# Performance work log

Hardware: AMD Instinct MI355X
Metric: run time of the kernel (lower is better)

The kernel has to match this reference:

```python
import jax, jax.numpy as jnp
import numpy as np

N_HEAD = 16
N_EMBD = 1024
TIME_EMBD = 64
EPS = 1e-5

def _ln(x, w, b):
    mu = jnp.mean(x, axis=-1, keepdims=True)
    var = jnp.mean(jnp.square(x - mu), axis=-1, keepdims=True)
    return (x - mu) * jax.lax.rsqrt(var + EPS) * w + b

def _gelu(x):
    return jax.nn.gelu(x, approximate=False)

def setup_inputs() -> dict:
    key = jax.random.key(0)
    ks = jax.random.split(key, 12)
    B, T, D, TE = 2, 2048, N_EMBD, TIME_EMBD
    C = D + TE  # 1088
    s = lambda fan_in: 1.0 / np.sqrt(fan_in)
    return {
        "z": jax.random.normal(ks[0], (B, T, D), jnp.float32),
        "t": jax.random.uniform(ks[1], (B,), jnp.float32),
        # time_mlp: Linear(1, TE) -> GELU -> Linear(TE, TE)
        "w_t1": jax.random.normal(ks[2], (1, TE), jnp.float32) * s(1),
        "b_t1": jnp.zeros((TE,), jnp.float32),
        "w_t2": jax.random.normal(ks[3], (TE, TE), jnp.float32) * s(TE),
        "b_t2": jnp.zeros((TE,), jnp.float32),
        # attention
        "ln_a_w": jnp.ones((C,), jnp.float32),
        "ln_a_b": jnp.zeros((C,), jnp.float32),
        "w_attn": jax.random.normal(ks[4], (C, 3 * D), jnp.float32) * s(C),
        "b_attn": jnp.zeros((3 * D,), jnp.float32),
        "w_proj": jax.random.normal(ks[5], (D, D), jnp.float32) * s(D),
        "b_proj": jnp.zeros((D,), jnp.float32),
        # mlp
        "ln_m_w": jnp.ones((C,), jnp.float32),
        "ln_m_b": jnp.zeros((C,), jnp.float32),
        "w_fc": jax.random.normal(ks[6], (C, 4 * D), jnp.float32) * s(C),
        "b_fc": jnp.zeros((4 * D,), jnp.float32),
        "w_fc2": jax.random.normal(ks[7], (4 * D, D), jnp.float32) * s(4 * D),
        "b_fc2": jnp.zeros((D,), jnp.float32),
    }

def reference(z, t, w_t1, b_t1, w_t2, b_t2, ln_a_w, ln_a_b, w_attn, b_attn,
              w_proj, b_proj, ln_m_w, ln_m_b, w_fc, b_fc, w_fc2, b_fc2):
    B, T, D = z.shape
    H, hd = N_HEAD, N_EMBD // N_HEAD
    # time embedding: [B, TE] broadcast over T
    t_emb = _gelu(t[:, None] @ w_t1 + b_t1) @ w_t2 + b_t2
    t_emb_bt = jnp.broadcast_to(t_emb[:, None, :], (B, T, TIME_EMBD))
    # --- attention with time-conditioned input ---
    zt = jnp.concatenate([z, t_emb_bt], axis=-1)            # [B,T,D+TE]
    x = _ln(zt, ln_a_w, ln_a_b)
    qkv = x @ w_attn + b_attn                               # [B,T,3D]
    q, k, v = jnp.split(qkv, 3, axis=-1)
    q = q.reshape(B, T, H, hd)
    k = k.reshape(B, T, H, hd)
    v = v.reshape(B, T, H, hd)
    att = jnp.einsum('bqhd,bkhd->bhqk', q, k) * (1.0 / np.sqrt(hd))
    mask = jnp.tril(jnp.ones((T, T), bool))
    att = jnp.where(mask, att, -jnp.inf)
    att = jax.nn.softmax(att, axis=-1)
    y = jnp.einsum('bhqk,bkhd->bqhd', att, v).reshape(B, T, D)
    h = y @ w_proj + b_proj                                 # [B,T,D]
    # --- mlp with time-conditioned input ---
    ht = jnp.concatenate([h, t_emb_bt], axis=-1)
    m = _ln(ht, ln_m_w, ln_m_b)
    dz = _gelu(m @ w_fc + b_fc) @ w_fc2 + b_fc2             # [B,T,D]
    return dz
```

## Files before the change

kernel.cpp:

```cpp
#include <hip/hip_runtime.h>
#include <stdint.h>
#include <math.h>

#define T_SEQ 2048
#define NHEAD 16
#define HD 64
#define DMODEL 1024
#define CDIM 1088
#define MROWS 4096

typedef uint16_t u16;
typedef __bf16 b8v __attribute__((ext_vector_type(8)));
typedef float f4v __attribute__((ext_vector_type(4)));

typedef __attribute__((address_space(3))) void lds_void;
typedef const __attribute__((address_space(1))) void glb_void;

__device__ __forceinline__ float b2f(u16 u) {
  union { uint32_t i; float f; } c; c.i = ((uint32_t)u) << 16; return c.f;
}
__device__ __forceinline__ u16 f2b(float f) {
  union { float f; uint32_t i; } c; c.f = f;
  uint32_t x = c.i;
  return (u16)((x + 0x7fffu + ((x >> 16) & 1u)) >> 16);
}
__device__ __forceinline__ float gelu_f(float x) {
  float ax = fabsf(x);
  float xs = ax * 0.70710678118654752f;
  float t = __frcp_rn(1.0f + 0.3275911f * xs);
  float poly = ((((1.061405429f * t - 1.453152027f) * t + 1.421413741f) * t
                 - 0.284496736f) * t + 0.254829592f) * t;
  float e = __expf(-xs * xs);
  float er = 1.0f - poly * e;
  er = copysignf(er, x);
  return 0.5f * x * (1.0f + er);
}

__global__ void time_mlp_kernel(const float* __restrict__ t, const float* __restrict__ w1,
                                const float* __restrict__ b1, const float* __restrict__ w2,
                                const float* __restrict__ b2, float* __restrict__ temb) {
  __shared__ float h1[2][64];
  int tid = threadIdx.x;
  int b = tid >> 6, i = tid & 63;
  float tv = t[b];
  h1[b][i] = gelu_f(tv * w1[i] + b1[i]);
  __syncthreads();
  float acc = b2[i];
  for (int k = 0; k < 64; ++k) acc += h1[b][k] * w2[k * 64 + i];
  temb[b * 64 + i] = acc;
}

__global__ __launch_bounds__(256) void transpose_kernel(const float* __restrict__ src,
                                                        u16* __restrict__ dst,
                                                        int R, int C) {
  __shared__ u16 tile[32][33];
  int tx = threadIdx.x & 31, ty = threadIdx.x >> 5;
  int c0 = blockIdx.x * 32, r0 = blockIdx.y * 32;
#pragma unroll
  for (int i = 0; i < 4; ++i) {
    int r = ty + i * 8;
    tile[r][tx] = f2b(src[(size_t)(r0 + r) * C + c0 + tx]);
  }
  __syncthreads();
#pragma unroll
  for (int i = 0; i < 4; ++i) {
    int c = ty + i * 8;
    dst[(size_t)(c0 + c) * R + r0 + tx] = tile[tx][c];
  }
}

__global__ __launch_bounds__(256) void add2_kernel(const float4* __restrict__ a,
                                                   const float4* __restrict__ b,
                                                   float4* __restrict__ o, int n4) {
  int i = blockIdx.x * 256 + threadIdx.x;
  if (i < n4) {
    float4 x = a[i], y = b[i];
    o[i] = float4{x.x + y.x, x.y + y.y, x.z + y.z, x.w + y.w};
  }
}

__global__ __launch_bounds__(256) void ln_concat_kernel(const float* __restrict__ zf,
                                                        const float* __restrict__ zf2,
                                                        const u16* __restrict__ zb,
                                                        const float* __restrict__ temb,
                                                        const float* __restrict__ w,
                                                        const float* __restrict__ bvec,
                                                        u16* __restrict__ xout,
                                                        int mode) {
  __shared__ float red[4];
  int row = blockIdx.x;
  int b = row / T_SEQ;
  int tid = threadIdx.x;
  float v[5];
  float sum = 0.f;
#pragma unroll
  for (int i = 0; i < 5; ++i) {
    int c = tid + i * 256;
    float val = 0.f;
    if (c < CDIM) {
      if (c < DMODEL) {
        size_t idx = (size_t)row * DMODEL + c;
        if (mode == 0) val = b2f(zb[idx]);
        else if (mode == 1) val = zf[idx];
        else val = zf[idx] + zf2[idx];
      } else {
        val = temb[b * 64 + (c - DMODEL)];
      }
    }
    v[i] = val;
    sum += val;
  }
#pragma unroll
  for (int off = 32; off; off >>= 1) sum += __shfl_xor(sum, off, 64);
  int wv = tid >> 6, ln = tid & 63;
  if (ln == 0) red[wv] = sum;
  __syncthreads();
  float mean = (red[0] + red[1] + red[2] + red[3]) * (1.0f / CDIM);
  __syncthreads();
  float sq = 0.f;
#pragma unroll
  for (int i = 0; i < 5; ++i) {
    int c = tid + i * 256;
    if (c < CDIM) { float d = v[i] - mean; sq += d * d; }
  }
#pragma unroll
  for (int off = 32; off; off >>= 1) sq += __shfl_xor(sq, off, 64);
  if (ln == 0) red[wv] = sq;
  __syncthreads();
  float inv = rsqrtf((red[0] + red[1] + red[2] + red[3]) * (1.0f / CDIM) + 1e-5f);
#pragma unroll
  for (int i = 0; i < 5; ++i) {
    int c = tid + i * 256;
    if (c < CDIM)
      xout[(size_t)row * CDIM + c] = f2b((v[i] - mean) * inv * w[c] + bvec[c]);
  }
}

__global__ __launch_bounds__(256) void gemm_bt_kernel(const u16* __restrict__ A,
                                                      const u16* __restrict__ Bt,
                                                      const float* __restrict__ bias,
                                                      void* __restrict__ Cout,
                                                      int M, int N, int K,
                                                      int do_gelu, int out_f32) {
  __shared__ u16 As[2][128 * 32];
  __shared__ u16 Bs[2][128 * 32];
  const int tid = threadIdx.x;
  const int wave = tid >> 6, lane = tid & 63;
  const int wr = wave >> 1, wc = wave & 1;
  const int m0 = blockIdx.x * 128;
  const int n0 = blockIdx.y * 128;
  const int lrow = lane & 15, quad = lane >> 4;
  const int srow = lane >> 2, sseg = lane & 3;

  const u16* gA0 = A  + (size_t)(m0 + wave * 32 + srow) * K + sseg * 8;
  const u16* gA1 = gA0 + (size_t)16 * K;
  const u16* gB0 = Bt + (size_t)(n0 + wave * 32 + srow) * K + sseg * 8;
  const u16* gB1 = gB0 + (size_t)16 * K;
  const int la0 = (wave * 32) * 32, la1 = (wave * 32 + 16) * 32;

  f4v acc[4][4] = {};

  __builtin_amdgcn_global_load_lds((glb_void*)gA0, (lds_void*)&As[0][la0], 16, 0, 0);
  __builtin_amdgcn_global_load_lds((glb_void*)gA1, (lds_void*)&As[0][la1], 16, 0, 0);
  __builtin_amdgcn_global_load_lds((glb_void*)gB0, (lds_void*)&Bs[0][la0], 16, 0, 0);
  __builtin_amdgcn_global_load_lds((glb_void*)gB1, (lds_void*)&Bs[0][la1], 16, 0, 0);

  int cur = 0;
  for (int k0 = 0; k0 < K; k0 += 32) {
    __syncthreads();
    if (k0 + 32 < K) {
      int nxt = cur ^ 1;
      __builtin_amdgcn_global_load_lds((glb_void*)(gA0 + k0 + 32), (lds_void*)&As[nxt][la0], 16, 0, 0);
      __builtin_amdgcn_global_load_lds((glb_void*)(gA1 + k0 + 32), (lds_void*)&As[nxt][la1], 16, 0, 0);
      __builtin_amdgcn_global_load_lds((glb_void*)(gB0 + k0 + 32), (lds_void*)&Bs[nxt][la0], 16, 0, 0);
      __builtin_amdgcn_global_load_lds((glb_void*)(gB1 + k0 + 32), (lds_void*)&Bs[nxt][la1], 16, 0, 0);
    }
    b8v af[4], bfr[4];
#pragma unroll
    for (int mi = 0; mi < 4; ++mi)
      af[mi] = *(const b8v*)(&As[cur][(wr * 64 + mi * 16 + lrow) * 32 + quad * 8]);
#pragma unroll
    for (int ni = 0; ni < 4; ++ni)
      bfr[ni] = *(const b8v*)(&Bs[cur][(wc * 64 + ni * 16 + lrow) * 32 + quad * 8]);
#pragma unroll
    for (int mi = 0; mi < 4; ++mi)
#pragma unroll
      for (int ni = 0; ni < 4; ++ni)
        acc[mi][ni] = __builtin_amdgcn_mfma_f32_16x16x32_bf16(bfr[ni], af[mi], acc[mi][ni], 0, 0, 0);
    cur ^= 1;
  }

#pragma unroll
  for (int mi = 0; mi < 4; ++mi) {
    int grow = m0 + wr * 64 + mi * 16 + lrow;
    size_t rb = (size_t)grow * N;
#pragma unroll
    for (int ni = 0; ni < 4; ++ni) {
      int gcol = n0 + wc * 64 + ni * 16 + quad * 4;
      float4 bv = *(const float4*)(bias + gcol);
      float v0 = acc[mi][ni][0] + bv.x;
      float v1 = acc[mi][ni][1] + bv.y;
      float v2 = acc[mi][ni][2] + bv.z;
      float v3 = acc[mi][ni][3] + bv.w;
      if (do_gelu) {
        v0 = gelu_f(v0); v1 = gelu_f(v1); v2 = gelu_f(v2); v3 = gelu_f(v3);
      }
      if (out_f32) {
        *(float4*)((float*)Cout + rb + gcol) = float4{v0, v1, v2, v3};
      } else {
        ushort4 ov;
        ov.x = f2b(v0); ov.y = f2b(v1); ov.z = f2b(v2); ov.w = f2b(v3);
        *(ushort4*)((u16*)Cout + rb + gcol) = ov;
      }
    }
  }
}

__global__ __launch_bounds__(256) void gemm_splitk2_kernel(const u16* __restrict__ A,
                                                           const u16* __restrict__ Bt,
                                                           const float* __restrict__ bias,
                                                           float* __restrict__ C0,
                                                           float* __restrict__ C1,
                                                           int M, int N, int K, int Kc) {
  __shared__ u16 As[2][128 * 32];
  __shared__ u16 Bs[2][128 * 32];
  const int tid = threadIdx.x;
  const int wave = tid >> 6, lane = tid & 63;
  const int wr = wave >> 1, wc = wave & 1;
  const int m0 = blockIdx.x * 128;
  const int n0 = blockIdx.y * 128;
  const int kz = blockIdx.z;
  const int lrow = lane & 15, quad = lane >> 4;
  const int srow = lane >> 2, sseg = lane & 3;

  const u16* gA0 = A  + (size_t)(m0 + wave * 32 + srow) * K + kz * Kc + sseg * 8;
  const u16* gA1 = gA0 + (size_t)16 * K;
  const u16* gB0 = Bt + (size_t)(n0 + wave * 32 + srow) * K + kz * Kc + sseg * 8;
  const u16* gB1 = gB0 + (size_t)16 * K;
  const int la0 = (wave * 32) * 32, la1 = (wave * 32 + 16) * 32;

  f4v acc[4][4] = {};

  __builtin_amdgcn_global_load_lds((glb_void*)gA0, (lds_void*)&As[0][la0], 16, 0, 0);
  __builtin_amdgcn_global_load_lds((glb_void*)gA1, (lds_void*)&As[0][la1], 16, 0, 0);
  __builtin_amdgcn_global_load_lds((glb_void*)gB0, (lds_void*)&Bs[0][la0], 16, 0, 0);
  __builtin_amdgcn_global_load_lds((glb_void*)gB1, (lds_void*)&Bs[0][la1], 16, 0, 0);

  int cur = 0;
  for (int k0 = 0; k0 < Kc; k0 += 32) {
    __syncthreads();
    if (k0 + 32 < Kc) {
      int nxt = cur ^ 1;
      __builtin_amdgcn_global_load_lds((glb_void*)(gA0 + k0 + 32), (lds_void*)&As[nxt][la0], 16, 0, 0);
      __builtin_amdgcn_global_load_lds((glb_void*)(gA1 + k0 + 32), (lds_void*)&As[nxt][la1], 16, 0, 0);
      __builtin_amdgcn_global_load_lds((glb_void*)(gB0 + k0 + 32), (lds_void*)&Bs[nxt][la0], 16, 0, 0);
      __builtin_amdgcn_global_load_lds((glb_void*)(gB1 + k0 + 32), (lds_void*)&Bs[nxt][la1], 16, 0, 0);
    }
    b8v af[4], bfr[4];
#pragma unroll
    for (int mi = 0; mi < 4; ++mi)
      af[mi] = *(const b8v*)(&As[cur][(wr * 64 + mi * 16 + lrow) * 32 + quad * 8]);
#pragma unroll
    for (int ni = 0; ni < 4; ++ni)
      bfr[ni] = *(const b8v*)(&Bs[cur][(wc * 64 + ni * 16 + lrow) * 32 + quad * 8]);
#pragma unroll
    for (int mi = 0; mi < 4; ++mi)
#pragma unroll
      for (int ni = 0; ni < 4; ++ni)
        acc[mi][ni] = __builtin_amdgcn_mfma_f32_16x16x32_bf16(bfr[ni], af[mi], acc[mi][ni], 0, 0, 0);
    cur ^= 1;
  }

  float* C = kz ? C1 : C0;
#pragma unroll
  for (int mi = 0; mi < 4; ++mi) {
    int grow = m0 + wr * 64 + mi * 16 + lrow;
    size_t rb = (size_t)grow * N;
#pragma unroll
    for (int ni = 0; ni < 4; ++ni) {
      int gcol = n0 + wc * 64 + ni * 16 + quad * 4;
      float4 bv;
      if (kz == 0) bv = *(const float4*)(bias + gcol);
      else bv = float4{0.f, 0.f, 0.f, 0.f};
      *(float4*)(C + rb + gcol) = float4{acc[mi][ni][0] + bv.x, acc[mi][ni][1] + bv.y,
                                         acc[mi][ni][2] + bv.z, acc[mi][ni][3] + bv.w};
    }
  }
}

__global__ __launch_bounds__(256) void attn_mfma_kernel(const u16* __restrict__ qkv,
                                                        u16* __restrict__ y) {
  __shared__ u16 Ks[64 * 72];
  __shared__ u16 Vts[64 * 72];
  __shared__ u16 Ps[64 * 72];
  const int bh = blockIdx.x;
  const int b = bh >> 4, h = bh & 15;
  const int qt = 31 - blockIdx.y;
  const int tid = threadIdx.x, w = tid >> 6, lane = tid & 63;
  const int lrow = lane & 15, quad = lane >> 4;
  const int q0 = qt * 64;
  const int qg = q0 + w * 16 + lrow;

  b8v qf[2];
#pragma unroll
  for (int dc = 0; dc < 2; ++dc)
    qf[dc] = *(const b8v*)(qkv + (size_t)(b * T_SEQ + qg) * 3072 + h * 64 + dc * 32 + quad * 8);

  f4v oacc[4] = {};
  float mrun = -__builtin_inff(), lrun = 0.f;

  const int nch = qt + 1;
  for (int ct = 0; ct < nch; ++ct) {
    __syncthreads();
    {
      int r = tid >> 2, sg = tid & 3;
      const u16* src = qkv + (size_t)(b * T_SEQ + ct * 64 + r) * 3072 + h * 64 + 1024 + sg * 16;
      *(uint4*)(&Ks[r * 72 + sg * 16]) = *(const uint4*)(src);
      *(uint4*)(&Ks[r * 72 + sg * 16 + 8]) = *(const uint4*)(src + 8);
    }
    {
      int pr = tid >> 3, dsg = tid & 7;
      const u16* v0 = qkv + (size_t)(b * T_SEQ + ct * 64 + 2 * pr) * 3072 + h * 64 + 2048 + dsg * 8;
      uint4 a = *(const uint4*)(v0);
      uint4 bb = *(const uint4*)(v0 + 3072);
      uint32_t aw[4] = {a.x, a.y, a.z, a.w};
      uint32_t bw[4] = {bb.x, bb.y, bb.z, bb.w};
#pragma unroll
      for (int j = 0; j < 8; ++j) {
        int d = dsg * 8 + j;
        u16 ae = (u16)(aw[j >> 1] >> ((j & 1) * 16));
        u16 be = (u16)(bw[j >> 1] >> ((j & 1) * 16));
        int keyp = (2 * pr) ^ (((d >> 3) & 7) * 8);
        *(uint32_t*)(&Vts[d * 72 + keyp]) = (uint32_t)ae | ((uint32_t)be << 16);
      }
    }
    __syncthreads();

    f4v sacc[4] = {};
#pragma unroll
    for (int ks = 0; ks < 4; ++ks)
#pragma unroll
      for (int dc = 0; dc < 2; ++dc) {
        b8v kf = *(const b8v*)(&Ks[(ks * 16 + lrow) * 72 + dc * 32 + quad * 8]);
        sacc[ks] = __builtin_amdgcn_mfma_f32_16x16x32_bf16(kf, qf[dc], sacc[ks], 0, 0, 0);
      }

    bool diag = (ct == qt);
#pragma unroll
    for (int ks = 0; ks < 4; ++ks)
#pragma unroll
      for (int r = 0; r < 4; ++r) {
        float v = sacc[ks][r] * 0.125f;
        int key = ct * 64 + ks * 16 + quad * 4 + r;
        if (diag && key > qg) v = -__builtin_inff();
        sacc[ks][r] = v;
      }

    float rmax = sacc[0][0];
#pragma unroll
    for (int ks = 0; ks < 4; ++ks)
#pragma unroll
      for (int r = 0; r < 4; ++r) rmax = fmaxf(rmax, sacc[ks][r]);
    rmax = fmaxf(rmax, __shfl_xor(rmax, 16, 64));
    rmax = fmaxf(rmax, __shfl_xor(rmax, 32, 64));
    float mn = fmaxf(mrun, rmax);
    float al = __expf(mrun - mn);
    mrun = mn;
    float psum = 0.f;
#pragma unroll
    for (int ks = 0; ks < 4; ++ks)
#pragma unroll
      for (int r = 0; r < 4; ++r) {
        float p = __expf(sacc[ks][r] - mn);
        sacc[ks][r] = p;
        psum += p;
      }
    psum += __shfl_xor(psum, 16, 64);
    psum += __shfl_xor(psum, 32, 64);
    lrun = lrun * al + psum;
#pragma unroll
    for (int ds = 0; ds < 4; ++ds) oacc[ds] *= al;

#pragma unroll
    for (int ks = 0; ks < 4; ++ks) {
      ushort4 pw;
      pw.x = f2b(sacc[ks][0]); pw.y = f2b(sacc[ks][1]);
      pw.z = f2b(sacc[ks][2]); pw.w = f2b(sacc[ks][3]);
      *(ushort4*)(&Ps[(w * 16 + lrow) * 72 + ks * 16 + quad * 4]) = pw;
    }

    b8v pf[2];
#pragma unroll
    for (int kc = 0; kc < 2; ++kc)
      pf[kc] = *(const b8v*)(&Ps[(w * 16 + lrow) * 72 + kc * 32 + quad * 8]);
#pragma unroll
    for (int ds = 0; ds < 4; ++ds)
#pragma unroll
      for (int kc = 0; kc < 2; ++kc) {
        int d = ds * 16 + lrow;
        int off = (kc * 32 + quad * 8) ^ (((d >> 3) & 7) * 8);
        b8v vfv = *(const b8v*)(&Vts[d * 72 + off]);
        oacc[ds] = __builtin_amdgcn_mfma_f32_16x16x32_bf16(vfv, pf[kc], oacc[ds], 0, 0, 0);
      }
  }

  float rinv = 1.0f / lrun;
  u16* yrow = y + (size_t)(b * T_SEQ + qg) * DMODEL + h * 64;
#pragma unroll
  for (int ds = 0; ds < 4; ++ds) {
    ushort4 ov;
    ov.x = f2b(oacc[ds][0] * rinv);
    ov.y = f2b(oacc[ds][1] * rinv);
    ov.z = f2b(oacc[ds][2] * rinv);
    ov.w = f2b(oacc[ds][3] * rinv);
    *(ushort4*)(yrow + ds * 16 + quad * 4) = ov;
  }
}

extern "C" void kernel_launch(void* const* d_in, const int* in_sizes, int n_in,
                              void* d_out, int out_size, void* d_ws, size_t ws_size,
                              hipStream_t stream) {
  const float* z      = (const float*)d_in[0];
  const float* t      = (const float*)d_in[1];
  const float* w_t1   = (const float*)d_in[2];
  const float* b_t1   = (const float*)d_in[3];
  const float* w_t2   = (const float*)d_in[4];
  const float* b_t2   = (const float*)d_in[5];
  const float* ln_a_w = (const float*)d_in[6];
  const float* ln_a_b = (const float*)d_in[7];
  const float* w_attn = (const float*)d_in[8];
  const float* b_attn = (const float*)d_in[9];
  const float* w_proj = (const float*)d_in[10];
  const float* b_proj = (const float*)d_in[11];
  const float* ln_m_w = (const float*)d_in[12];
  const float* ln_m_b = (const float*)d_in[13];
  const float* w_fc   = (const float*)d_in[14];
  const float* b_fc   = (const float*)d_in[15];
  const float* w_fc2  = (const float*)d_in[16];
  const float* b_fc2  = (const float*)d_in[17];

  char* ws = (char*)d_ws;
  float* temb  = (float*)ws;
  u16* wT_attn = (u16*)(ws + 1024);
  u16* wT_proj = wT_attn + (size_t)3072 * 1088;
  u16* wT_fc   = wT_proj + (size_t)1024 * 1024;
  u16* wT_fc2  = wT_fc   + (size_t)4096 * 1088;
  u16* xbuf    = wT_fc2  + (size_t)1024 * 4096;
  u16* big     = xbuf    + (size_t)4096 * 1088;
  u16* ybuf    = big     + (size_t)4096 * 4096;
  float* p0    = (float*)(ybuf + (size_t)4096 * 1024);
  float* p1    = p0 + (size_t)4096 * 1024;

  time_mlp_kernel<<<dim3(1), dim3(128), 0, stream>>>(t, w_t1, b_t1, w_t2, b_t2, temb);

  transpose_kernel<<<dim3(3072 / 32, 1088 / 32), dim3(256), 0, stream>>>(w_attn, wT_attn, 1088, 3072);
  transpose_kernel<<<dim3(1024 / 32, 1024 / 32), dim3(256), 0, stream>>>(w_proj, wT_proj, 1024, 1024);
  transpose_kernel<<<dim3(4096 / 32, 1088 / 32), dim3(256), 0, stream>>>(w_fc, wT_fc, 1088, 4096);
  transpose_kernel<<<dim3(1024 / 32, 4096 / 32), dim3(256), 0, stream>>>(w_fc2, wT_fc2, 4096, 1024);

  ln_concat_kernel<<<dim3(MROWS), dim3(256), 0, stream>>>(
      z, (const float*)nullptr, (const u16*)nullptr, temb, ln_a_w, ln_a_b, xbuf, 1);

  gemm_bt_kernel<<<dim3(MROWS / 128, 3072 / 128), dim3(256), 0, stream>>>(
      xbuf, wT_attn, b_attn, big, MROWS, 3072, 1088, 0, 0);

  attn_mfma_kernel<<<dim3(32, 32), dim3(256), 0, stream>>>(big, ybuf);

  gemm_splitk2_kernel<<<dim3(MROWS / 128, 1024 / 128, 2), dim3(256), 0, stream>>>(
      ybuf, wT_proj, b_proj, p0, p1, MROWS, 1024, 1024, 512);

  ln_concat_kernel<<<dim3(MROWS), dim3(256), 0, stream>>>(
      p0, p1, (const u16*)nullptr, temb, ln_m_w, ln_m_b, xbuf, 2);

  gemm_bt_kernel<<<dim3(MROWS / 128, 4096 / 128), dim3(256), 0, stream>>>(
      xbuf, wT_fc, b_fc, big, MROWS, 4096, 1088, 1, 0);

  gemm_splitk2_kernel<<<dim3(MROWS / 128, 1024 / 128, 2), dim3(256), 0, stream>>>(
      big, wT_fc2, b_fc2, p0, p1, MROWS, 1024, 4096, 2048);

  add2_kernel<<<dim3((MROWS * 1024 / 4 + 255) / 256), dim3(256), 0, stream>>>(
      (const float4*)p0, (const float4*)p1, (float4*)d_out, MROWS * 1024 / 4);
}
```

Baseline: 395.9 us.

## Replace 128x128 GEMM with 256x256 swizzled 8-wave pipelined GEMM and split-K4 FC2

Replaces the 128x128 bt GEMM with a 256x256-tile, 512-thread kernel used for the QKV, FC and FC2 GEMMs. The new kernel uses a K step of 64, an XOR-swizzled LDS layout, and staged global-to-LDS loads interleaved with MFMA phases under s_setprio. It also remaps block IDs so neighbouring blocks share operand tiles in cache. FC2 moves from split-K 2 to split-K 4, reusing the transposed attention-weight buffer and the output as partial-sum storage, followed by a 4-way add. The intent is more data reuse per tile and more overlap of loads with math, at the cost of more LDS and registers per block and an extra partial-sum buffer to read back.

```diff
diff --git a/kernel.cpp b/kernel.cpp
--- a/kernel.cpp
+++ b/kernel.cpp
@@ -15,6 +15,8 @@
 
 typedef __attribute__((address_space(3))) void lds_void;
 typedef const __attribute__((address_space(1))) void glb_void;
+
+#define GLL(g, l) __builtin_amdgcn_global_load_lds((glb_void*)(g), (lds_void*)(l), 16, 0, 0)
 
 __device__ __forceinline__ float b2f(u16 u) {
   union { uint32_t i; float f; } c; c.i = ((uint32_t)u) << 16; return c.f;
@@ -69,19 +71,21 @@
   }
 }
 
-__global__ __launch_bounds__(256) void add2_kernel(const float4* __restrict__ a,
+__global__ __launch_bounds__(256) void add4_kernel(const float4* __restrict__ a,
                                                    const float4* __restrict__ b,
+                                                   const float4* __restrict__ c,
+                                                   const float4* __restrict__ d,
                                                    float4* __restrict__ o, int n4) {
   int i = blockIdx.x * 256 + threadIdx.x;
   if (i < n4) {
-    float4 x = a[i], y = b[i];
-    o[i] = float4{x.x + y.x, x.y + y.y, x.z + y.z, x.w + y.w};
+    float4 x = a[i], y = b[i], z = c[i], w = d[i];
+    o[i] = float4{x.x + y.x + z.x + w.x, x.y + y.y + z.y + w.y,
+                  x.z + y.z + z.z + w.z, x.w + y.w + z.w + w.w};
   }
 }
 
 __global__ __launch_bounds__(256) void ln_concat_kernel(const float* __restrict__ zf,
                                                         const float* __restrict__ zf2,
-                                                        const u16* __restrict__ zb,
                                                         const float* __restrict__ temb,
                                                         const float* __restrict__ w,
                                                         const float* __restrict__ bvec,
@@ -100,8 +104,7 @@
     if (c < CDIM) {
       if (c < DMODEL) {
         size_t idx = (size_t)row * DMODEL + c;
-        if (mode == 0) val = b2f(zb[idx]);
-        else if (mode == 1) val = zf[idx];
+        if (mode == 1) val = zf[idx];
         else val = zf[idx] + zf2[idx];
       } else {
         val = temb[b * 64 + (c - DMODEL)];
@@ -136,84 +139,161 @@
   }
 }
 
-__global__ __launch_bounds__(256) void gemm_bt_kernel(const u16* __restrict__ A,
-                                                      const u16* __restrict__ Bt,
-                                                      const float* __restrict__ bias,
-                                                      void* __restrict__ Cout,
-                                                      int M, int N, int K,
-                                                      int do_gelu, int out_f32) {
-  __shared__ u16 As[2][128 * 32];
-  __shared__ u16 Bs[2][128 * 32];
+__global__ __launch_bounds__(512, 2) void gemm256_kernel(
+    const u16* __restrict__ A, const u16* __restrict__ Bt,
+    const float* __restrict__ bias,
+    void* __restrict__ c0, void* __restrict__ c1,
+    void* __restrict__ c2, void* __restrict__ c3,
+    int M, int N, int K, int k_tiles, int do_gelu, int out_f32) {
+  __shared__ u16 As[2][256 * 64];
+  __shared__ u16 Bs[2][256 * 64];
   const int tid = threadIdx.x;
   const int wave = tid >> 6, lane = tid & 63;
-  const int wr = wave >> 1, wc = wave & 1;
-  const int m0 = blockIdx.x * 128;
-  const int n0 = blockIdx.y * 128;
+  const int wr = wave >> 2, wc = wave & 3;
   const int lrow = lane & 15, quad = lane >> 4;
-  const int srow = lane >> 2, sseg = lane & 3;
-
-  const u16* gA0 = A  + (size_t)(m0 + wave * 32 + srow) * K + sseg * 8;
-  const u16* gA1 = gA0 + (size_t)16 * K;
-  const u16* gB0 = Bt + (size_t)(n0 + wave * 32 + srow) * K + sseg * 8;
-  const u16* gB1 = gB0 + (size_t)16 * K;
-  const int la0 = (wave * 32) * 32, la1 = (wave * 32 + 16) * 32;
-
-  f4v acc[4][4] = {};
-
-  __builtin_amdgcn_global_load_lds((glb_void*)gA0, (lds_void*)&As[0][la0], 16, 0, 0);
-  __builtin_amdgcn_global_load_lds((glb_void*)gA1, (lds_void*)&As[0][la1], 16, 0, 0);
-  __builtin_amdgcn_global_load_lds((glb_void*)gB0, (lds_void*)&Bs[0][la0], 16, 0, 0);
-  __builtin_amdgcn_global_load_lds((glb_void*)gB1, (lds_void*)&Bs[0][la1], 16, 0, 0);
-
-  int cur = 0;
-  for (int k0 = 0; k0 < K; k0 += 32) {
-    __syncthreads();
-    if (k0 + 32 < K) {
-      int nxt = cur ^ 1;
-      __builtin_amdgcn_global_load_lds((glb_void*)(gA0 + k0 + 32), (lds_void*)&As[nxt][la0], 16, 0, 0);
-      __builtin_amdgcn_global_load_lds((glb_void*)(gA1 + k0 + 32), (lds_void*)&As[nxt][la1], 16, 0, 0);
-      __builtin_amdgcn_global_load_lds((glb_void*)(gB0 + k0 + 32), (lds_void*)&Bs[nxt][la0], 16, 0, 0);
-      __builtin_amdgcn_global_load_lds((glb_void*)(gB1 + k0 + 32), (lds_void*)&Bs[nxt][la1], 16, 0, 0);
-    }
-    b8v af[4], bfr[4];
-#pragma unroll
-    for (int mi = 0; mi < 4; ++mi)
-      af[mi] = *(const b8v*)(&As[cur][(wr * 64 + mi * 16 + lrow) * 32 + quad * 8]);
-#pragma unroll
-    for (int ni = 0; ni < 4; ++ni)
-      bfr[ni] = *(const b8v*)(&Bs[cur][(wc * 64 + ni * 16 + lrow) * 32 + quad * 8]);
-#pragma unroll
-    for (int mi = 0; mi < 4; ++mi)
-#pragma unroll
-      for (int ni = 0; ni < 4; ++ni)
-        acc[mi][ni] = __builtin_amdgcn_mfma_f32_16x16x32_bf16(bfr[ni], af[mi], acc[mi][ni], 0, 0, 0);
-    cur ^= 1;
-  }
-
-#pragma unroll
-  for (int mi = 0; mi < 4; ++mi) {
-    int grow = m0 + wr * 64 + mi * 16 + lrow;
-    size_t rb = (size_t)grow * N;
-#pragma unroll
-    for (int ni = 0; ni < 4; ++ni) {
-      int gcol = n0 + wc * 64 + ni * 16 + quad * 4;
-      float4 bv = *(const float4*)(bias + gcol);
-      float v0 = acc[mi][ni][0] + bv.x;
-      float v1 = acc[mi][ni][1] + bv.y;
-      float v2 = acc[mi][ni][2] + bv.z;
-      float v3 = acc[mi][ni][3] + bv.w;
-      if (do_gelu) {
-        v0 = gelu_f(v0); v1 = gelu_f(v1); v2 = gelu_f(v2); v3 = gelu_f(v3);
-      }
-      if (out_f32) {
-        *(float4*)((float*)Cout + rb + gcol) = float4{v0, v1, v2, v3};
-      } else {
-        ushort4 ov;
-        ov.x = f2b(v0); ov.y = f2b(v1); ov.z = f2b(v2); ov.w = f2b(v3);
-        *(ushort4*)((u16*)Cout + rb + gcol) = ov;
-      }
-    }
-  }
+
+  int nxy = gridDim.x * gridDim.y;
+  int bid = blockIdx.y * gridDim.x + blockIdx.x;
+  int cpx = nxy >> 3;
+  int swz = (bid & 7) * cpx + (bid >> 3);
+  int bx = swz % gridDim.x, by = swz / gridDim.x;
+  const int m0 = bx * 256, n0 = by * 256;
+  const int kz = blockIdx.z;
+  const int kb = kz * k_tiles * 64;
+  const int NT = k_tiles;
+
+  const int sr = tid >> 3;
+  const int sc = ((tid & 7) ^ ((tid >> 3) & 7)) * 8;
+  const u16* gA = A + (size_t)(m0 + sr) * K + kb + sc;
+  const u16* gB = Bt + (size_t)(n0 + sr) * K + kb + sc;
+
+  f4v acc[8][4] = {};
+  b8v bq[2][4];
+
+  auto STAGE_A = [&](int t, int h) {
+    const u16* g = gA + (size_t)(h * 128) * K + t * 64;
+    u16* l = (u16*)As[t & 1] + h * 8192 + (wave << 9);
+    GLL(g, l);
+    GLL(g + (size_t)64 * K, l + 4096);
+  };
+  auto STAGE_B = [&](int t, int h) {
+    const u16* g = gB + (size_t)(h * 128) * K + t * 64;
+    u16* l = (u16*)Bs[t & 1] + h * 8192 + (wave << 9);
+    GLL(g, l);
+    GLL(g + (size_t)64 * K, l + 4096);
+  };
+
+  STAGE_A(0, 0); STAGE_A(0, 1); STAGE_B(0, 0); STAGE_B(0, 1);
+  if (NT > 1) {
+    STAGE_A(1, 0);
+    asm volatile("s_waitcnt vmcnt(2)" ::: "memory");
+  } else {
+    asm volatile("s_waitcnt vmcnt(0)" ::: "memory");
+  }
+  __builtin_amdgcn_s_barrier();
+
+  for (int t = 0; t < NT; ++t) {
+    const char* abase = (const char*)As[t & 1];
+    const char* bbase = (const char*)Bs[t & 1];
+    const int asw = (lrow & 7) << 4;
+    b8v af[4];
+
+#pragma unroll
+    for (int j = 0; j < 4; ++j)
+      af[j] = *(const b8v*)(abase + (j * 32 + wr * 16 + lrow) * 128 + ((quad * 16) ^ asw));
+#pragma unroll
+    for (int n = 0; n < 4; ++n)
+      bq[0][n] = *(const b8v*)(bbase + (wc * 64 + n * 16 + lrow) * 128 + ((quad * 16) ^ asw));
+    if (t + 1 < NT) STAGE_A(t + 1, 1);
+    __builtin_amdgcn_s_barrier();
+    __builtin_amdgcn_s_setprio(1);
+#pragma unroll
+    for (int j = 0; j < 4; ++j)
+#pragma unroll
+      for (int n = 0; n < 4; ++n)
+        acc[j][n] = __builtin_amdgcn_mfma_f32_16x16x32_bf16(bq[0][n], af[j], acc[j][n], 0, 0, 0);
+    __builtin_amdgcn_s_setprio(0);
+    __builtin_amdgcn_s_barrier();
+
+#pragma unroll
+    for (int j = 0; j < 4; ++j)
+      af[j] = *(const b8v*)(abase + (j * 32 + wr * 16 + lrow) * 128 + ((64 + quad * 16) ^ asw));
+#pragma unroll
+    for (int n = 0; n < 4; ++n)
+      bq[1][n] = *(const b8v*)(bbase + (wc * 64 + n * 16 + lrow) * 128 + ((64 + quad * 16) ^ asw));
+    if (t + 1 < NT) STAGE_B(t + 1, 0);
+    __builtin_amdgcn_s_barrier();
+    __builtin_amdgcn_s_setprio(1);
+#pragma unroll
+    for (int j = 0; j < 4; ++j)
+#pragma unroll
+      for (int n = 0; n < 4; ++n)
+        acc[j][n] = __builtin_amdgcn_mfma_f32_16x16x32_bf16(bq[1][n], af[j], acc[j][n], 0, 0, 0);
+    __builtin_amdgcn_s_setprio(0);
+    __builtin_amdgcn_s_barrier();
+
+#pragma unroll
+    for (int j = 0; j < 4; ++j)
+      af[j] = *(const b8v*)(abase + (128 + j * 32 + wr * 16 + lrow) * 128 + ((quad * 16) ^ asw));
+    if (t + 1 < NT) STAGE_B(t + 1, 1);
+    __builtin_amdgcn_s_barrier();
+    __builtin_amdgcn_s_setprio(1);
+#pragma unroll
+    for (int j = 0; j < 4; ++j)
+#pragma unroll
+      for (int n = 0; n < 4; ++n)
+        acc[4 + j][n] = __builtin_amdgcn_mfma_f32_16x16x32_bf16(bq[0][n], af[j], acc[4 + j][n], 0, 0, 0);
+    __builtin_amdgcn_s_setprio(0);
+    __builtin_amdgcn_s_barrier();
+
+#pragma unroll
+    for (int j = 0; j < 4; ++j)
+      af[j] = *(const b8v*)(abase + (128 + j * 32 + wr * 16 + lrow) * 128 + ((64 + quad * 16) ^ asw));
+    if (t + 2 < NT) STAGE_A(t + 2, 0);
+    __builtin_amdgcn_s_barrier();
+    __builtin_amdgcn_s_setprio(1);
+#pragma unroll
+    for (int j = 0; j < 4; ++j)
+#pragma unroll
+      for (int n = 0; n < 4; ++n)
+        acc[4 + j][n] = __builtin_amdgcn_mfma_f32_16x16x32_bf16(bq[1][n], af[j], acc[4 + j][n], 0, 0, 0);
+    __builtin_amdgcn_s_setprio(0);
+    if (t + 1 < NT) {
+      if (t + 2 < NT) asm volatile("s_waitcnt vmcnt(2)" ::: "memory");
+      else            asm volatile("s_waitcnt vmcnt(0)" ::: "memory");
+    }
+    __builtin_amdgcn_s_barrier();
+  }
+
+  void* Cout = (kz == 0) ? c0 : (kz == 1) ? c1 : (kz == 2) ? c2 : c3;
+#pragma unroll
+  for (int mh = 0; mh < 2; ++mh)
+#pragma unroll
+    for (int j = 0; j < 4; ++j) {
+      int grow = m0 + mh * 128 + j * 32 + wr * 16 + lrow;
+      size_t rb = (size_t)grow * N;
+#pragma unroll
+      for (int n = 0; n < 4; ++n) {
+        int gcol = n0 + wc * 64 + n * 16 + quad * 4;
+        float b0 = 0.f, b1 = 0.f, b2 = 0.f, b3 = 0.f;
+        if (kz == 0) {
+          float4 bv = *(const float4*)(bias + gcol);
+          b0 = bv.x; b1 = bv.y; b2 = bv.z; b3 = bv.w;
+        }
+        f4v a = acc[mh * 4 + j][n];
+        float v0 = a[0] + b0, v1 = a[1] + b1, v2 = a[2] + b2, v3 = a[3] + b3;
+        if (do_gelu) {
+          v0 = gelu_f(v0); v1 = gelu_f(v1); v2 = gelu_f(v2); v3 = gelu_f(v3);
+        }
+        if (out_f32) {
+          *(float4*)((float*)Cout + rb + gcol) = float4{v0, v1, v2, v3};
+        } else {
+          ushort4 ov;
+          ov.x = f2b(v0); ov.y = f2b(v1); ov.z = f2b(v2); ov.w = f2b(v3);
+          *(ushort4*)((u16*)Cout + rb + gcol) = ov;
+        }
+      }
+    }
 }
 
 __global__ __launch_bounds__(256) void gemm_splitk2_kernel(const u16* __restrict__ A,
@@ -241,20 +321,16 @@
 
   f4v acc[4][4] = {};
 
-  __builtin_amdgcn_global_load_lds((glb_void*)gA0, (lds_void*)&As[0][la0], 16, 0, 0);
-  __builtin_amdgcn_global_load_lds((glb_void*)gA1, (lds_void*)&As[0][la1], 16, 0, 0);
-  __builtin_amdgcn_global_load_lds((glb_void*)gB0, (lds_void*)&Bs[0][la0], 16, 0, 0);
-  __builtin_amdgcn_global_load_lds((glb_void*)gB1, (lds_void*)&Bs[0][la1], 16, 0, 0);
+  GLL(gA0, &As[0][la0]); GLL(gA1, &As[0][la1]);
+  GLL(gB0, &Bs[0][la0]); GLL(gB1, &Bs[0][la1]);
 
   int cur = 0;
   for (int k0 = 0; k0 < Kc; k0 += 32) {
     __syncthreads();
     if (k0 + 32 < Kc) {
       int nxt = cur ^ 1;
-      __builtin_amdgcn_global_load_lds((glb_void*)(gA0 + k0 + 32), (lds_void*)&As[nxt][la0], 16, 0, 0);
-      __builtin_amdgcn_global_load_lds((glb_void*)(gA1 + k0 + 32), (lds_void*)&As[nxt][la1], 16, 0, 0);
-      __builtin_amdgcn_global_load_lds((glb_void*)(gB0 + k0 + 32), (lds_void*)&Bs[nxt][la0], 16, 0, 0);
-      __builtin_amdgcn_global_load_lds((glb_void*)(gB1 + k0 + 32), (lds_void*)&Bs[nxt][la1], 16, 0, 0);
+      GLL(gA0 + k0 + 32, &As[nxt][la0]); GLL(gA1 + k0 + 32, &As[nxt][la1]);
+      GLL(gB0 + k0 + 32, &Bs[nxt][la0]); GLL(gB1 + k0 + 32, &Bs[nxt][la1]);
     }
     b8v af[4], bfr[4];
 #pragma unroll
@@ -279,11 +355,13 @@
 #pragma unroll
     for (int ni = 0; ni < 4; ++ni) {
       int gcol = n0 + wc * 64 + ni * 16 + quad * 4;
-      float4 bv;
-      if (kz == 0) bv = *(const float4*)(bias + gcol);
-      else bv = float4{0.f, 0.f, 0.f, 0.f};
-      *(float4*)(C + rb + gcol) = float4{acc[mi][ni][0] + bv.x, acc[mi][ni][1] + bv.y,
-                                         acc[mi][ni][2] + bv.z, acc[mi][ni][3] + bv.w};
+      float b0 = 0.f, b1 = 0.f, b2 = 0.f, b3 = 0.f;
+      if (kz == 0) {
+        float4 bv = *(const float4*)(bias + gcol);
+        b0 = bv.x; b1 = bv.y; b2 = bv.z; b3 = bv.w;
+      }
+      *(float4*)(C + rb + gcol) = float4{acc[mi][ni][0] + b0, acc[mi][ni][1] + b1,
+                                         acc[mi][ni][2] + b2, acc[mi][ni][3] + b3};
     }
   }
 }
@@ -450,6 +528,7 @@
   u16* ybuf    = big     + (size_t)4096 * 4096;
   float* p0    = (float*)(ybuf + (size_t)4096 * 1024);
   float* p1    = p0 + (size_t)4096 * 1024;
+  float* p3    = (float*)wT_attn;
 
   time_mlp_kernel<<<dim3(1), dim3(128), 0, stream>>>(t, w_t1, b_t1, w_t2, b_t2, temb);
 
@@ -459,10 +538,11 @@
   transpose_kernel<<<dim3(1024 / 32, 4096 / 32), dim3(256), 0, stream>>>(w_fc2, wT_fc2, 4096, 1024);
 
   ln_concat_kernel<<<dim3(MROWS), dim3(256), 0, stream>>>(
-      z, (const float*)nullptr, (const u16*)nullptr, temb, ln_a_w, ln_a_b, xbuf, 1);
-
-  gemm_bt_kernel<<<dim3(MROWS / 128, 3072 / 128), dim3(256), 0, stream>>>(
-      xbuf, wT_attn, b_attn, big, MROWS, 3072, 1088, 0, 0);
+      z, (const float*)nullptr, temb, ln_a_w, ln_a_b, xbuf, 1);
+
+  gemm256_kernel<<<dim3(16, 12, 1), dim3(512), 0, stream>>>(
+      xbuf, wT_attn, b_attn, big, nullptr, nullptr, nullptr,
+      MROWS, 3072, 1088, 17, 0, 0);
 
   attn_mfma_kernel<<<dim3(32, 32), dim3(256), 0, stream>>>(big, ybuf);
 
@@ -470,14 +550,17 @@
       ybuf, wT_proj, b_proj, p0, p1, MROWS, 1024, 1024, 512);
 
   ln_concat_kernel<<<dim3(MROWS), dim3(256), 0, stream>>>(
-      p0, p1, (const u16*)nullptr, temb, ln_m_w, ln_m_b, xbuf, 2);
-
-  gemm_bt_kernel<<<dim3(MROWS / 128, 4096 / 128), dim3(256), 0, stream>>>(
-      xbuf, wT_fc, b_fc, big, MROWS, 4096, 1088, 1, 0);
-
-  gemm_splitk2_kernel<<<dim3(MROWS / 128, 1024 / 128, 2), dim3(256), 0, stream>>>(
-      big, wT_fc2, b_fc2, p0, p1, MROWS, 1024, 4096, 2048);
-
-  add2_kernel<<<dim3((MROWS * 1024 / 4 + 255) / 256), dim3(256), 0, stream>>>(
-      (const float4*)p0, (const float4*)p1, (float4*)d_out, MROWS * 1024 / 4);
-}
+      p0, p1, temb, ln_m_w, ln_m_b, xbuf, 2);
+
+  gemm256_kernel<<<dim3(16, 16, 1), dim3(512), 0, stream>>>(
+      xbuf, wT_fc, b_fc, big, nullptr, nullptr, nullptr,
+      MROWS, 4096, 1088, 17, 1, 0);
+
+  gemm256_kernel<<<dim3(16, 4, 4), dim3(512), 0, stream>>>(
+      big, wT_fc2, b_fc2, p0, p1, d_out, p3,
+      MROWS, 1024, 4096, 16, 0, 1);
+
+  add4_kernel<<<dim3(MROWS * 1024 / 4 / 256), dim3(256), 0, stream>>>(
+      (const float4*)p0, (const float4*)p1, (const float4*)d_out, (const float4*)p3,
+      (float4*)d_out, MROWS * 1024 / 4);
+}
```

After: 385.3 us. 2.7% less time.
